# Kernel optimization log

Hardware: AMD Instinct MI355X
Metric: run time of the kernel (lower is better)

Reference implementation:

```python
import jax, jax.numpy as jnp
from jax import lax
import numpy as np

B, L, E, H = 4, 512, 1024, 128


def setup_inputs() -> dict:
    key = jax.random.key(0)
    k0, k1, k2, k3, k4, k5 = jax.random.split(key, 6)
    s = 1.0 / np.sqrt(E)
    return {
        "rec_emb": jax.random.normal(k0, (B, L, E), jnp.float32),
        "lig_emb": jax.random.normal(k1, (B, L, E), jnp.float32),
        "W1": jax.random.normal(k2, (E, H), jnp.float32) * s,
        "b1": jax.random.normal(k3, (H,), jnp.float32) * 0.01,
        "conv_w": jax.random.normal(k4, (1, H, 2, 2), jnp.float32) * (1.0 / np.sqrt(H * 4)),
        "conv_b": jax.random.normal(k5, (1,), jnp.float32) * 0.01,
    }


def reference(rec_emb, lig_emb, W1, b1, conv_w, conv_b):
    # shared fc: Linear -> ReLU (Dropout is identity in eval mode)
    rec_hid = jax.nn.relu(jnp.einsum("bie,eh->bih", rec_emb, W1) + b1)
    lig_hid = jax.nn.relu(jnp.einsum("bje,eh->bjh", lig_emb, W1) + b1)
    # outer-product bilinear map: bih,bjh->bijh, then tanh
    mat = jnp.tanh(rec_hid[:, :, None, :] * lig_hid[:, None, :, :])
    # permute to NCHW: (b, h, i, j)
    mat = jnp.transpose(mat, (0, 3, 1, 2))
    # Conv2d(H -> 1, kernel=2, padding=1): out spatial = L + 1
    y = lax.conv_general_dilated(
        mat, conv_w, window_strides=(1, 1), padding=[(1, 1), (1, 1)],
        dimension_numbers=("NCHW", "OIHW", "NCHW"),
    ) + conv_b[None, :, None, None]
    # MaxPool2d(kernel=2, stride=2), floor mode
    pooled = lax.reduce_window(
        y, -jnp.inf, lax.max,
        window_dimensions=(1, 1, 2, 2), window_strides=(1, 1, 2, 2),
        padding="VALID",
    )
    # global max over spatial dims -> (b, 1), sigmoid, flatten
    m = jnp.max(pooled, axis=(2, 3))
    return jax.nn.sigmoid(m).reshape(-1)
```

## Files before the change

### kernel.cpp

```cpp
#include <hip/hip_runtime.h>
#include <hip/hip_fp16.h>
#include <math.h>

#define BDIM 4
#define LDIM 512
#define EDIM 1024
#define HDIM 128
#define TILE 32
#define NT   16
#define K2   2.885390081777927f

typedef unsigned short ushort_t;
typedef __attribute__((ext_vector_type(8))) _Float16 half8;
typedef __attribute__((ext_vector_type(4))) float f32x4;

struct __align__(16) H8 { __half2 p[4]; };
union HU { H8 h; half8 v; };

__global__ __launch_bounds__(256) void gemm_direct(
    const float* __restrict__ rec, const float* __restrict__ lig,
    const float* __restrict__ W1, const float* __restrict__ b1,
    const float* __restrict__ cw, ushort_t* __restrict__ hid,
    ushort_t* __restrict__ wneg, float* __restrict__ wsumg) {
  if (blockIdx.x == 512) {
    __shared__ float wp[2][4];
    const int t = threadIdx.x;
    if (t < HDIM) {
      float4 w4 = *(const float4*)&cw[t * 4];
      _Float16 h0 = (_Float16)(-2.f * w4.x), h1 = (_Float16)(-2.f * w4.y);
      _Float16 h2 = (_Float16)(-2.f * w4.z), h3 = (_Float16)(-2.f * w4.w);
      wneg[0 * HDIM + t] = *(ushort_t*)&h0;
      wneg[1 * HDIM + t] = *(ushort_t*)&h1;
      wneg[2 * HDIM + t] = *(ushort_t*)&h2;
      wneg[3 * HDIM + t] = *(ushort_t*)&h3;
#pragma unroll
      for (int k = 4; k < 16; ++k) wneg[k * HDIM + t] = 0;
      float4 ws = w4;
#pragma unroll
      for (int off = 32; off > 0; off >>= 1) {
        ws.x += __shfl_down(ws.x, off, 64);
        ws.y += __shfl_down(ws.y, off, 64);
        ws.z += __shfl_down(ws.z, off, 64);
        ws.w += __shfl_down(ws.w, off, 64);
      }
      if ((t & 63) == 0) {
        wp[t >> 6][0] = ws.x; wp[t >> 6][1] = ws.y;
        wp[t >> 6][2] = ws.z; wp[t >> 6][3] = ws.w;
      }
    }
    __syncthreads();
    if (t < 4) wsumg[t] = wp[0][t] + wp[1][t];
    return;
  }

  const int gw = (int)blockIdx.x * 4 + (threadIdx.x >> 6);
  const int l = threadIdx.x & 63;
  const int strip = gw >> 3;
  const int nidx = gw & 7;
  const int r0 = strip * 16;
  const int m = l & 15, q = l >> 4;
  const float* arow = ((r0 < BDIM * LDIM)
                           ? rec + (size_t)r0 * EDIM
                           : lig + (size_t)(r0 - BDIM * LDIM) * EDIM) +
                      (size_t)m * EDIM + q * 8;
  const int col = nidx * 16 + m;
  const float* wcol = W1 + col;

  f32x4 acc = {0.f, 0.f, 0.f, 0.f};
  for (int blk = 0; blk < 8; ++blk) {
    float4 alo[4], ahi[4];
    float bw[4][8];
#pragma unroll
    for (int j = 0; j < 4; ++j) {
      const int k0 = (blk * 4 + j) * 32 + q * 8;
      alo[j] = *(const float4*)(arow + (blk * 4 + j) * 32);
      ahi[j] = *(const float4*)(arow + (blk * 4 + j) * 32 + 4);
#pragma unroll
      for (int kk = 0; kk < 8; ++kk)
        bw[j][kk] = wcol[(size_t)(k0 + kk) * HDIM];
    }
#pragma unroll
    for (int j = 0; j < 4; ++j) {
      HU au, bu;
      au.h.p[0] = __floats2half2_rn(alo[j].x, alo[j].y);
      au.h.p[1] = __floats2half2_rn(alo[j].z, alo[j].w);
      au.h.p[2] = __floats2half2_rn(ahi[j].x, ahi[j].y);
      au.h.p[3] = __floats2half2_rn(ahi[j].z, ahi[j].w);
      bu.h.p[0] = __floats2half2_rn(bw[j][0], bw[j][1]);
      bu.h.p[1] = __floats2half2_rn(bw[j][2], bw[j][3]);
      bu.h.p[2] = __floats2half2_rn(bw[j][4], bw[j][5]);
      bu.h.p[3] = __floats2half2_rn(bw[j][6], bw[j][7]);
      acc = __builtin_amdgcn_mfma_f32_16x16x32_f16(au.v, bu.v, acc, 0, 0, 0);
    }
  }
  const float scale = (r0 < BDIM * LDIM) ? -K2 : 1.0f;
  const float bias = b1[col];
#pragma unroll
  for (int r = 0; r < 4; ++r) {
    float v = fmaxf(acc[r] + bias, 0.f) * scale;
    ((_Float16*)hid)[(size_t)(r0 + q * 4 + r) * HDIM + col] = (_Float16)v;
  }
}

__global__ __launch_bounds__(256, 4) void bilinear_max(
    const ushort_t* __restrict__ hid, const ushort_t* __restrict__ wneg,
    const float* __restrict__ wsumg, const float* __restrict__ cw,
    const float* __restrict__ cb, float* __restrict__ partial) {
  __shared__ ushort_t rl[33][130];
  __shared__ ushort_t ll[33][130];
  __shared__ ushort_t sl4[33][34][4];
  __shared__ float wred[4];

  const int t = threadIdx.x;
  const int b = blockIdx.z;
  const int ib = (int)blockIdx.y * TILE - 1;
  const int jb = (int)blockIdx.x * TILE - 1;
  const int w = t >> 6, l = t & 63;
  const int q = l >> 4, c15 = l & 15;

  half8 wf[4];
#pragma unroll
  for (int c = 0; c < 4; ++c)
    wf[c] = *(const half8*)&wneg[c15 * HDIM + c * 32 + q * 8];
  const float wsum_v = (c15 < 4) ? wsumg[c15] : 0.f;

  H8 z;
  z.p[0] = z.p[1] = z.p[2] = z.p[3] = __floats2half2_rn(0.f, 0.f);
  for (int p = t; p < 66 * 16; p += 256) {
    int r = p >> 4, seg = (p & 15) * 8;
    if (r < 33) {
      int i = ib + r;
      H8 v = z;
      if (i >= 0) v = *(const H8*)&hid[((size_t)(b * LDIM + i)) * HDIM + seg];
      *(H8*)&rl[r][seg] = v;
    } else {
      int j = jb + (r - 33);
      H8 v = z;
      if (j >= 0) v = *(const H8*)&hid[((size_t)((BDIM + b) * LDIM + j)) * HDIM + seg];
      *(H8*)&ll[r - 33][seg] = v;
    }
  }
  __syncthreads();

  const __half2 E0 = __float2half2_rn(0.991381f);
  const __half2 E1 = __float2half2_rn(-0.818328f);
  const __half2 E2 = __float2half2_rn(0.333048f);
#define POLYG(U) __hmul2(U, __hfma2(U, __hfma2(U, E2, E1), E0))
#define GCHAIN(GU, RU, LU)                                                    \
  {                                                                           \
    __half2 u0 = h2exp2(__hmul2((RU).h.p[0], (LU).h.p[0]));                   \
    __half2 u1 = h2exp2(__hmul2((RU).h.p[1], (LU).h.p[1]));                   \
    __half2 u2 = h2exp2(__hmul2((RU).h.p[2], (LU).h.p[2]));                   \
    __half2 u3 = h2exp2(__hmul2((RU).h.p[3], (LU).h.p[3]));                   \
    (GU).h.p[0] = POLYG(u0);                                                  \
    (GU).h.p[1] = POLYG(u1);                                                  \
    (GU).h.p[2] = POLYG(u2);                                                  \
    (GU).h.p[3] = POLYG(u3);                                                  \
  }

#pragma unroll
  for (int hf = 0; hf < 2; ++hf) {
    const int jj0 = hf << 4;
    HU lu[4];
#pragma unroll
    for (int c = 0; c < 4; ++c)
      lu[c].v = *(const half8*)&ll[jj0 + c15][c * 32 + q * 8];
#pragma unroll
    for (int ii4 = 0; ii4 < 2; ++ii4) {
      const int ii = w * 8 + ii4 * 4;
      f32x4 a0 = {0.f, 0.f, 0.f, 0.f}, a1 = a0, a2 = a0, a3 = a0;
#pragma unroll
      for (int c = 0; c < 4; ++c) {
        HU r0, r1, r2, r3, g0, g1, g2, g3;
        r0.v = *(const half8*)&rl[ii + 0][c * 32 + q * 8];
        r1.v = *(const half8*)&rl[ii + 1][c * 32 + q * 8];
        r2.v = *(const half8*)&rl[ii + 2][c * 32 + q * 8];
        r3.v = *(const half8*)&rl[ii + 3][c * 32 + q * 8];
        GCHAIN(g0, r0, lu[c])
        GCHAIN(g1, r1, lu[c])
        GCHAIN(g2, r2, lu[c])
        GCHAIN(g3, r3, lu[c])
        a0 = __builtin_amdgcn_mfma_f32_16x16x32_f16(g0.v, wf[c], a0, 0, 0, 0);
        a1 = __builtin_amdgcn_mfma_f32_16x16x32_f16(g1.v, wf[c], a1, 0, 0, 0);
        a2 = __builtin_amdgcn_mfma_f32_16x16x32_f16(g2.v, wf[c], a2, 0, 0, 0);
        a3 = __builtin_amdgcn_mfma_f32_16x16x32_f16(g3.v, wf[c], a3, 0, 0, 0);
      }
      if (c15 < 4) {
#pragma unroll
        for (int r = 0; r < 4; ++r) {
          _Float16 h0 = (_Float16)(wsum_v + a0[r]);
          _Float16 h1 = (_Float16)(wsum_v + a1[r]);
          _Float16 h2 = (_Float16)(wsum_v + a2[r]);
          _Float16 h3 = (_Float16)(wsum_v + a3[r]);
          sl4[ii + 0][jj0 + q * 4 + r][c15] = *(ushort_t*)&h0;
          sl4[ii + 1][jj0 + q * 4 + r][c15] = *(ushort_t*)&h1;
          sl4[ii + 2][jj0 + q * 4 + r][c15] = *(ushort_t*)&h2;
          sl4[ii + 3][jj0 + q * 4 + r][c15] = *(ushort_t*)&h3;
        }
      }
    }
  }
#undef GCHAIN

  if (t < 130) {
    const int pr = t >> 1;
    const int hh = (t & 1) * 64;
    const int pi = (pr < 33) ? pr : 32;
    const int qj = (pr < 33) ? 32 : (pr - 33);
    float sa0 = 0.f, sa1 = 0.f, sa2 = 0.f, sa3 = 0.f;
    for (int h8 = hh; h8 < hh + 64; h8 += 8) {
      HU r8, l8;
      r8.v = *(const half8*)&rl[pi][h8];
      l8.v = *(const half8*)&ll[qj][h8];
#pragma unroll
      for (int j = 0; j < 4; ++j) {
        float2 pf = __half22float2(__hmul2(r8.h.p[j], l8.h.p[j]));
        float u0 = __builtin_amdgcn_exp2f(pf.x);
        float u1 = __builtin_amdgcn_exp2f(pf.y);
        float g0 = u0 * fmaf(u0, fmaf(u0, 0.333048f, -0.818328f), 0.991381f);
        float g1 = u1 * fmaf(u1, fmaf(u1, 0.333048f, -0.818328f), 0.991381f);
        float4 wa = *(const float4*)&cw[(h8 + 2 * j) * 4];
        float4 wb = *(const float4*)&cw[(h8 + 2 * j + 1) * 4];
        sa0 = fmaf(-2.f * g0, wa.x, fmaf(-2.f * g1, wb.x, sa0));
        sa1 = fmaf(-2.f * g0, wa.y, fmaf(-2.f * g1, wb.y, sa1));
        sa2 = fmaf(-2.f * g0, wa.z, fmaf(-2.f * g1, wb.z, sa2));
        sa3 = fmaf(-2.f * g0, wa.w, fmaf(-2.f * g1, wb.w, sa3));
      }
    }
    sa0 += __shfl_xor(sa0, 1, 64);
    sa1 += __shfl_xor(sa1, 1, 64);
    sa2 += __shfl_xor(sa2, 1, 64);
    sa3 += __shfl_xor(sa3, 1, 64);
    if ((t & 1) == 0) {
      _Float16 h0 = (_Float16)(wsumg[0] + sa0);
      _Float16 h1 = (_Float16)(wsumg[1] + sa1);
      _Float16 h2 = (_Float16)(wsumg[2] + sa2);
      _Float16 h3 = (_Float16)(wsumg[3] + sa3);
      sl4[pi][qj][0] = *(ushort_t*)&h0;
      sl4[pi][qj][1] = *(ushort_t*)&h1;
      sl4[pi][qj][2] = *(ushort_t*)&h2;
      sl4[pi][qj][3] = *(ushort_t*)&h3;
    }
  }
  __syncthreads();

  float m = -INFINITY;
  const float cbv = cb[0];
  for (int p = t; p < 1024; p += 256) {
    int jj = (p & 31) + 1, iy = (p >> 5) + 1;
    float v = cbv + (float)(*(const _Float16*)&sl4[iy - 1][jj - 1][0])
                  + (float)(*(const _Float16*)&sl4[iy - 1][jj][1])
                  + (float)(*(const _Float16*)&sl4[iy][jj - 1][2])
                  + (float)(*(const _Float16*)&sl4[iy][jj][3]);
    m = fmaxf(m, v);
  }
#pragma unroll
  for (int off = 32; off > 0; off >>= 1) m = fmaxf(m, __shfl_down(m, off, 64));
  if ((t & 63) == 0) wred[t >> 6] = m;
  __syncthreads();
  if (t == 0) {
    float mm = fmaxf(fmaxf(wred[0], wred[1]), fmaxf(wred[2], wred[3]));
    partial[((size_t)b * NT + blockIdx.y) * NT + blockIdx.x] = mm;
  }
}

__global__ __launch_bounds__(64) void finalize(const float* __restrict__ partial,
                                               float* __restrict__ out) {
  const int b = blockIdx.x, t = threadIdx.x;
  float m = -INFINITY;
  for (int p = t; p < NT * NT; p += 64) m = fmaxf(m, partial[b * NT * NT + p]);
#pragma unroll
  for (int off = 32; off > 0; off >>= 1) m = fmaxf(m, __shfl_down(m, off, 64));
  if (t == 0) out[b] = 1.f / (1.f + expf(-m));
}

extern "C" void kernel_launch(void* const* d_in, const int* in_sizes, int n_in,
                              void* d_out, int out_size, void* d_ws, size_t ws_size,
                              hipStream_t stream) {
  const float* rec = (const float*)d_in[0];
  const float* lig = (const float*)d_in[1];
  const float* W1  = (const float*)d_in[2];
  const float* b1  = (const float*)d_in[3];
  const float* cw  = (const float*)d_in[4];
  const float* cb  = (const float*)d_in[5];
  float* out = (float*)d_out;

  ushort_t* hid  = (ushort_t*)d_ws;
  float* partial = (float*)(hid + (size_t)2 * BDIM * LDIM * HDIM);
  ushort_t* wneg = (ushort_t*)(partial + NT * NT * BDIM);
  float* wsumg   = (float*)(wneg + 16 * HDIM);

  gemm_direct<<<dim3(513), 256, 0, stream>>>(rec, lig, W1, b1, cw, hid, wneg, wsumg);
  bilinear_max<<<dim3(NT, NT, BDIM), 256, 0, stream>>>(hid, wneg, wsumg, cw, cb, partial);
  finalize<<<dim3(BDIM), 64, 0, stream>>>(partial, out);
}
```

Baseline: 122.2 us.

## Pretranspose W1 to fp16 and shrink bilinear tile to 16x32 for occupancy

Adds a prep kernel that converts W1 to a transposed fp16 layout once per call, so the GEMM loads contiguous half8 vectors instead of eight strided fp32 loads per MFMA operand and drops the per-iteration conversions. The bilinear tile is reduced from 32x32 to 16x32 with launch bounds raised to 8 blocks per CU. The aim is more blocks and better occupancy, at the cost of more halo recomputation per output. This adds an extra kernel launch and reduces per-block reuse of the loaded row and column tiles.

New measurement: 128.1 us. 4.8% more time.

```diff
diff --git a/kernel.cpp b/kernel.cpp
--- a/kernel.cpp
+++ b/kernel.cpp
@@ -6,8 +6,10 @@
 #define LDIM 512
 #define EDIM 1024
 #define HDIM 128
-#define TILE 32
-#define NT   16
+#define TI   16
+#define TJ   32
+#define NTI  32
+#define NTJ  16
 #define K2   2.885390081777927f
 
 typedef unsigned short ushort_t;
@@ -17,14 +19,25 @@
 struct __align__(16) H8 { __half2 p[4]; };
 union HU { H8 h; half8 v; };
 
-__global__ __launch_bounds__(256) void gemm_direct(
-    const float* __restrict__ rec, const float* __restrict__ lig,
-    const float* __restrict__ W1, const float* __restrict__ b1,
-    const float* __restrict__ cw, ushort_t* __restrict__ hid,
-    ushort_t* __restrict__ wneg, float* __restrict__ wsumg) {
-  if (blockIdx.x == 512) {
+__global__ __launch_bounds__(256) void prep(
+    const float* __restrict__ W1, const float* __restrict__ cw,
+    ushort_t* __restrict__ w1t, ushort_t* __restrict__ wneg,
+    float* __restrict__ wsumg) {
+  const int t = threadIdx.x;
+  const int tid = (int)blockIdx.x * 256 + t;
+  const int col = tid & 127;
+  const int k8 = (tid >> 7) * 8;
+  HU hu;
+#pragma unroll
+  for (int e = 0; e < 4; ++e) {
+    float a = W1[(size_t)(k8 + 2 * e) * HDIM + col];
+    float b = W1[(size_t)(k8 + 2 * e + 1) * HDIM + col];
+    hu.h.p[e] = __floats2half2_rn(a, b);
+  }
+  *(half8*)&w1t[(size_t)col * EDIM + k8] = hu.v;
+
+  if (blockIdx.x == 0) {
     __shared__ float wp[2][4];
-    const int t = threadIdx.x;
     if (t < HDIM) {
       float4 w4 = *(const float4*)&cw[t * 4];
       _Float16 h0 = (_Float16)(-2.f * w4.x), h1 = (_Float16)(-2.f * w4.y);
@@ -50,9 +63,13 @@
     }
     __syncthreads();
     if (t < 4) wsumg[t] = wp[0][t] + wp[1][t];
-    return;
-  }
-
+  }
+}
+
+__global__ __launch_bounds__(256) void gemm_direct(
+    const float* __restrict__ rec, const float* __restrict__ lig,
+    const ushort_t* __restrict__ w1t, const float* __restrict__ b1,
+    ushort_t* __restrict__ hid) {
   const int gw = (int)blockIdx.x * 4 + (threadIdx.x >> 6);
   const int l = threadIdx.x & 63;
   const int strip = gw >> 3;
@@ -64,33 +81,27 @@
                            : lig + (size_t)(r0 - BDIM * LDIM) * EDIM) +
                       (size_t)m * EDIM + q * 8;
   const int col = nidx * 16 + m;
-  const float* wcol = W1 + col;
+  const ushort_t* wrow = w1t + (size_t)col * EDIM + q * 8;
 
   f32x4 acc = {0.f, 0.f, 0.f, 0.f};
+#pragma unroll 2
   for (int blk = 0; blk < 8; ++blk) {
     float4 alo[4], ahi[4];
-    float bw[4][8];
+    half8 bv[4];
 #pragma unroll
     for (int j = 0; j < 4; ++j) {
-      const int k0 = (blk * 4 + j) * 32 + q * 8;
       alo[j] = *(const float4*)(arow + (blk * 4 + j) * 32);
       ahi[j] = *(const float4*)(arow + (blk * 4 + j) * 32 + 4);
-#pragma unroll
-      for (int kk = 0; kk < 8; ++kk)
-        bw[j][kk] = wcol[(size_t)(k0 + kk) * HDIM];
+      bv[j] = *(const half8*)&wrow[(blk * 4 + j) * 32];
     }
 #pragma unroll
     for (int j = 0; j < 4; ++j) {
-      HU au, bu;
+      HU au;
       au.h.p[0] = __floats2half2_rn(alo[j].x, alo[j].y);
       au.h.p[1] = __floats2half2_rn(alo[j].z, alo[j].w);
       au.h.p[2] = __floats2half2_rn(ahi[j].x, ahi[j].y);
       au.h.p[3] = __floats2half2_rn(ahi[j].z, ahi[j].w);
-      bu.h.p[0] = __floats2half2_rn(bw[j][0], bw[j][1]);
-      bu.h.p[1] = __floats2half2_rn(bw[j][2], bw[j][3]);
-      bu.h.p[2] = __floats2half2_rn(bw[j][4], bw[j][5]);
-      bu.h.p[3] = __floats2half2_rn(bw[j][6], bw[j][7]);
-      acc = __builtin_amdgcn_mfma_f32_16x16x32_f16(au.v, bu.v, acc, 0, 0, 0);
+      acc = __builtin_amdgcn_mfma_f32_16x16x32_f16(au.v, bv[j], acc, 0, 0, 0);
     }
   }
   const float scale = (r0 < BDIM * LDIM) ? -K2 : 1.0f;
@@ -102,19 +113,19 @@
   }
 }
 
-__global__ __launch_bounds__(256, 4) void bilinear_max(
+__global__ __launch_bounds__(256, 8) void bilinear_max(
     const ushort_t* __restrict__ hid, const ushort_t* __restrict__ wneg,
     const float* __restrict__ wsumg, const float* __restrict__ cw,
     const float* __restrict__ cb, float* __restrict__ partial) {
-  __shared__ ushort_t rl[33][130];
-  __shared__ ushort_t ll[33][130];
-  __shared__ ushort_t sl4[33][34][4];
+  __shared__ ushort_t rl[TI + 1][130];
+  __shared__ ushort_t ll[TJ + 1][130];
+  __shared__ ushort_t sl4[TI + 1][TJ + 2][4];
   __shared__ float wred[4];
 
   const int t = threadIdx.x;
   const int b = blockIdx.z;
-  const int ib = (int)blockIdx.y * TILE - 1;
-  const int jb = (int)blockIdx.x * TILE - 1;
+  const int ib = (int)blockIdx.y * TI - 1;
+  const int jb = (int)blockIdx.x * TJ - 1;
   const int w = t >> 6, l = t & 63;
   const int q = l >> 4, c15 = l & 15;
 
@@ -126,18 +137,18 @@
 
   H8 z;
   z.p[0] = z.p[1] = z.p[2] = z.p[3] = __floats2half2_rn(0.f, 0.f);
-  for (int p = t; p < 66 * 16; p += 256) {
+  for (int p = t; p < (TI + TJ + 2) * 16; p += 256) {
     int r = p >> 4, seg = (p & 15) * 8;
-    if (r < 33) {
+    if (r < TI + 1) {
       int i = ib + r;
       H8 v = z;
       if (i >= 0) v = *(const H8*)&hid[((size_t)(b * LDIM + i)) * HDIM + seg];
       *(H8*)&rl[r][seg] = v;
     } else {
-      int j = jb + (r - 33);
+      int j = jb + (r - (TI + 1));
       H8 v = z;
       if (j >= 0) v = *(const H8*)&hid[((size_t)((BDIM + b) * LDIM + j)) * HDIM + seg];
-      *(H8*)&ll[r - 33][seg] = v;
+      *(H8*)&ll[r - (TI + 1)][seg] = v;
     }
   }
   __syncthreads();
@@ -165,48 +176,46 @@
 #pragma unroll
     for (int c = 0; c < 4; ++c)
       lu[c].v = *(const half8*)&ll[jj0 + c15][c * 32 + q * 8];
-#pragma unroll
-    for (int ii4 = 0; ii4 < 2; ++ii4) {
-      const int ii = w * 8 + ii4 * 4;
-      f32x4 a0 = {0.f, 0.f, 0.f, 0.f}, a1 = a0, a2 = a0, a3 = a0;
-#pragma unroll
-      for (int c = 0; c < 4; ++c) {
-        HU r0, r1, r2, r3, g0, g1, g2, g3;
-        r0.v = *(const half8*)&rl[ii + 0][c * 32 + q * 8];
-        r1.v = *(const half8*)&rl[ii + 1][c * 32 + q * 8];
-        r2.v = *(const half8*)&rl[ii + 2][c * 32 + q * 8];
-        r3.v = *(const half8*)&rl[ii + 3][c * 32 + q * 8];
-        GCHAIN(g0, r0, lu[c])
-        GCHAIN(g1, r1, lu[c])
-        GCHAIN(g2, r2, lu[c])
-        GCHAIN(g3, r3, lu[c])
-        a0 = __builtin_amdgcn_mfma_f32_16x16x32_f16(g0.v, wf[c], a0, 0, 0, 0);
-        a1 = __builtin_amdgcn_mfma_f32_16x16x32_f16(g1.v, wf[c], a1, 0, 0, 0);
-        a2 = __builtin_amdgcn_mfma_f32_16x16x32_f16(g2.v, wf[c], a2, 0, 0, 0);
-        a3 = __builtin_amdgcn_mfma_f32_16x16x32_f16(g3.v, wf[c], a3, 0, 0, 0);
+    const int ii = w * 4;
+    f32x4 a0 = {0.f, 0.f, 0.f, 0.f}, a1 = a0, a2 = a0, a3 = a0;
+#pragma unroll
+    for (int c = 0; c < 4; ++c) {
+      HU r0, r1, r2, r3, g0, g1, g2, g3;
+      r0.v = *(const half8*)&rl[ii + 0][c * 32 + q * 8];
+      r1.v = *(const half8*)&rl[ii + 1][c * 32 + q * 8];
+      r2.v = *(const half8*)&rl[ii + 2][c * 32 + q * 8];
+      r3.v = *(const half8*)&rl[ii + 3][c * 32 + q * 8];
+      GCHAIN(g0, r0, lu[c])
+      GCHAIN(g1, r1, lu[c])
+      GCHAIN(g2, r2, lu[c])
+      GCHAIN(g3, r3, lu[c])
+      a0 = __builtin_amdgcn_mfma_f32_16x16x32_f16(g0.v, wf[c], a0, 0, 0, 0);
+      a1 = __builtin_amdgcn_mfma_f32_16x16x32_f16(g1.v, wf[c], a1, 0, 0, 0);
+      a2 = __builtin_amdgcn_mfma_f32_16x16x32_f16(g2.v, wf[c], a2, 0, 0, 0);
+      a3 = __builtin_amdgcn_mfma_f32_16x16x32_f16(g3.v, wf[c], a3, 0, 0, 0);
+    }
+    if (c15 < 4) {
+#pragma unroll
+      for (int r = 0; r < 4; ++r) {
+        _Float16 h0 = (_Float16)(wsum_v + a0[r]);
+        _Float16 h1 = (_Float16)(wsum_v + a1[r]);
+        _Float16 h2 = (_Float16)(wsum_v + a2[r]);
+        _Float16 h3 = (_Float16)(wsum_v + a3[r]);
+        sl4[ii + 0][jj0 + q * 4 + r][c15] = *(ushort_t*)&h0;
+        sl4[ii + 1][jj0 + q * 4 + r][c15] = *(ushort_t*)&h1;
+        sl4[ii + 2][jj0 + q * 4 + r][c15] = *(ushort_t*)&h2;
+        sl4[ii + 3][jj0 + q * 4 + r][c15] = *(ushort_t*)&h3;
       }
-      if (c15 < 4) {
-#pragma unroll
-        for (int r = 0; r < 4; ++r) {
-          _Float16 h0 = (_Float16)(wsum_v + a0[r]);
-          _Float16 h1 = (_Float16)(wsum_v + a1[r]);
-          _Float16 h2 = (_Float16)(wsum_v + a2[r]);
-          _Float16 h3 = (_Float16)(wsum_v + a3[r]);
-          sl4[ii + 0][jj0 + q * 4 + r][c15] = *(ushort_t*)&h0;
-          sl4[ii + 1][jj0 + q * 4 + r][c15] = *(ushort_t*)&h1;
-          sl4[ii + 2][jj0 + q * 4 + r][c15] = *(ushort_t*)&h2;
-          sl4[ii + 3][jj0 + q * 4 + r][c15] = *(ushort_t*)&h3;
-        }
-      }
     }
   }
 #undef GCHAIN
-
-  if (t < 130) {
+#undef POLYG
+
+  if (t < 98) {
     const int pr = t >> 1;
     const int hh = (t & 1) * 64;
-    const int pi = (pr < 33) ? pr : 32;
-    const int qj = (pr < 33) ? 32 : (pr - 33);
+    const int pi = (pr < TI + 1) ? pr : TI;
+    const int qj = (pr < TI + 1) ? TJ : (pr - (TI + 1));
     float sa0 = 0.f, sa1 = 0.f, sa2 = 0.f, sa3 = 0.f;
     for (int h8 = hh; h8 < hh + 64; h8 += 8) {
       HU r8, l8;
@@ -246,7 +255,7 @@
 
   float m = -INFINITY;
   const float cbv = cb[0];
-  for (int p = t; p < 1024; p += 256) {
+  for (int p = t; p < TI * TJ; p += 256) {
     int jj = (p & 31) + 1, iy = (p >> 5) + 1;
     float v = cbv + (float)(*(const _Float16*)&sl4[iy - 1][jj - 1][0])
                   + (float)(*(const _Float16*)&sl4[iy - 1][jj][1])
@@ -260,7 +269,7 @@
   __syncthreads();
   if (t == 0) {
     float mm = fmaxf(fmaxf(wred[0], wred[1]), fmaxf(wred[2], wred[3]));
-    partial[((size_t)b * NT + blockIdx.y) * NT + blockIdx.x] = mm;
+    partial[((size_t)b * NTI + blockIdx.y) * NTJ + blockIdx.x] = mm;
   }
 }
 
@@ -268,7 +277,7 @@
                                                float* __restrict__ out) {
   const int b = blockIdx.x, t = threadIdx.x;
   float m = -INFINITY;
-  for (int p = t; p < NT * NT; p += 64) m = fmaxf(m, partial[b * NT * NT + p]);
+  for (int p = t; p < NTI * NTJ; p += 64) m = fmaxf(m, partial[b * NTI * NTJ + p]);
 #pragma unroll
   for (int off = 32; off > 0; off >>= 1) m = fmaxf(m, __shfl_down(m, off, 64));
   if (t == 0) out[b] = 1.f / (1.f + expf(-m));
@@ -287,10 +296,12 @@
 
   ushort_t* hid  = (ushort_t*)d_ws;
   float* partial = (float*)(hid + (size_t)2 * BDIM * LDIM * HDIM);
-  ushort_t* wneg = (ushort_t*)(partial + NT * NT * BDIM);
+  ushort_t* wneg = (ushort_t*)(partial + NTI * NTJ * BDIM);
   float* wsumg   = (float*)(wneg + 16 * HDIM);
-
-  gemm_direct<<<dim3(513), 256, 0, stream>>>(rec, lig, W1, b1, cw, hid, wneg, wsumg);
-  bilinear_max<<<dim3(NT, NT, BDIM), 256, 0, stream>>>(hid, wneg, wsumg, cw, cb, partial);
+  ushort_t* w1t  = (ushort_t*)(wsumg + 4);
+
+  prep<<<dim3(64), 256, 0, stream>>>(W1, cw, w1t, wneg, wsumg);
+  gemm_direct<<<dim3(512), 256, 0, stream>>>(rec, lig, w1t, b1, hid);
+  bilinear_max<<<dim3(NTJ, NTI, BDIM), 256, 0, stream>>>(hid, wneg, wsumg, cw, cb, partial);
   finalize<<<dim3(BDIM), 64, 0, stream>>>(partial, out);
 }
```

## Split GEMM K across warps and double bilinear block threads

Applied to the files above, without the earlier changes.

The projection GEMM now gives each block one 16x16 output tile and splits the K=1024 reduction across its four warps, combining the partial sums through shared memory. That quadruples the grid to 2048+1 blocks and shortens each warp's serial MFMA chain. The bilinear kernel moves to 512 threads per block, so each warp handles 4 rows instead of 8, and the border computation is split four ways with one packed 8-byte store. The trade is more parallelism and latency hiding against a shared-memory reduction and a barrier in the GEMM, plus register pressure from the higher launch bounds.

Result: slower. 128.1 us (+4.8%).

```diff
diff --git a/kernel.cpp b/kernel.cpp
--- a/kernel.cpp
+++ b/kernel.cpp
@@ -16,13 +16,14 @@
 
 struct __align__(16) H8 { __half2 p[4]; };
 union HU { H8 h; half8 v; };
-
-__global__ __launch_bounds__(256) void gemm_direct(
+struct __align__(8) US4 { ushort_t u[4]; };
+
+__global__ __launch_bounds__(256, 8) void gemm_direct(
     const float* __restrict__ rec, const float* __restrict__ lig,
     const float* __restrict__ W1, const float* __restrict__ b1,
     const float* __restrict__ cw, ushort_t* __restrict__ hid,
     ushort_t* __restrict__ wneg, float* __restrict__ wsumg) {
-  if (blockIdx.x == 512) {
+  if (blockIdx.x == 2048) {
     __shared__ float wp[2][4];
     const int t = threadIdx.x;
     if (t < HDIM) {
@@ -53,63 +54,66 @@
     return;
   }
 
-  const int gw = (int)blockIdx.x * 4 + (threadIdx.x >> 6);
-  const int l = threadIdx.x & 63;
-  const int strip = gw >> 3;
-  const int nidx = gw & 7;
+  __shared__ float red[4][64][4];
+  const int t = threadIdx.x;
+  const int w = t >> 6, l = t & 63;
+  const int m = l & 15, q = l >> 4;
+  const int strip = (int)blockIdx.x >> 3;
+  const int nidx = (int)blockIdx.x & 7;
   const int r0 = strip * 16;
-  const int m = l & 15, q = l >> 4;
   const float* arow = ((r0 < BDIM * LDIM)
                            ? rec + (size_t)r0 * EDIM
                            : lig + (size_t)(r0 - BDIM * LDIM) * EDIM) +
-                      (size_t)m * EDIM + q * 8;
+                      (size_t)m * EDIM;
   const int col = nidx * 16 + m;
   const float* wcol = W1 + col;
+  const int ks = w * 256;
 
   f32x4 acc = {0.f, 0.f, 0.f, 0.f};
+#pragma unroll 2
   for (int blk = 0; blk < 8; ++blk) {
-    float4 alo[4], ahi[4];
-    float bw[4][8];
-#pragma unroll
-    for (int j = 0; j < 4; ++j) {
-      const int k0 = (blk * 4 + j) * 32 + q * 8;
-      alo[j] = *(const float4*)(arow + (blk * 4 + j) * 32);
-      ahi[j] = *(const float4*)(arow + (blk * 4 + j) * 32 + 4);
-#pragma unroll
-      for (int kk = 0; kk < 8; ++kk)
-        bw[j][kk] = wcol[(size_t)(k0 + kk) * HDIM];
-    }
-#pragma unroll
-    for (int j = 0; j < 4; ++j) {
-      HU au, bu;
-      au.h.p[0] = __floats2half2_rn(alo[j].x, alo[j].y);
-      au.h.p[1] = __floats2half2_rn(alo[j].z, alo[j].w);
-      au.h.p[2] = __floats2half2_rn(ahi[j].x, ahi[j].y);
-      au.h.p[3] = __floats2half2_rn(ahi[j].z, ahi[j].w);
-      bu.h.p[0] = __floats2half2_rn(bw[j][0], bw[j][1]);
-      bu.h.p[1] = __floats2half2_rn(bw[j][2], bw[j][3]);
-      bu.h.p[2] = __floats2half2_rn(bw[j][4], bw[j][5]);
-      bu.h.p[3] = __floats2half2_rn(bw[j][6], bw[j][7]);
-      acc = __builtin_amdgcn_mfma_f32_16x16x32_f16(au.v, bu.v, acc, 0, 0, 0);
-    }
-  }
-  const float scale = (r0 < BDIM * LDIM) ? -K2 : 1.0f;
-  const float bias = b1[col];
-#pragma unroll
-  for (int r = 0; r < 4; ++r) {
-    float v = fmaxf(acc[r] + bias, 0.f) * scale;
-    ((_Float16*)hid)[(size_t)(r0 + q * 4 + r) * HDIM + col] = (_Float16)v;
+    const int k0 = ks + blk * 32 + q * 8;
+    float4 alo = *(const float4*)(arow + k0);
+    float4 ahi = *(const float4*)(arow + k0 + 4);
+    float bw[8];
+#pragma unroll
+    for (int kk = 0; kk < 8; ++kk) bw[kk] = wcol[(size_t)(k0 + kk) * HDIM];
+    HU au, bu;
+    au.h.p[0] = __floats2half2_rn(alo.x, alo.y);
+    au.h.p[1] = __floats2half2_rn(alo.z, alo.w);
+    au.h.p[2] = __floats2half2_rn(ahi.x, ahi.y);
+    au.h.p[3] = __floats2half2_rn(ahi.z, ahi.w);
+    bu.h.p[0] = __floats2half2_rn(bw[0], bw[1]);
+    bu.h.p[1] = __floats2half2_rn(bw[2], bw[3]);
+    bu.h.p[2] = __floats2half2_rn(bw[4], bw[5]);
+    bu.h.p[3] = __floats2half2_rn(bw[6], bw[7]);
+    acc = __builtin_amdgcn_mfma_f32_16x16x32_f16(au.v, bu.v, acc, 0, 0, 0);
+  }
+  *(f32x4*)&red[w][l][0] = acc;
+  __syncthreads();
+  if (w == 0) {
+    f32x4 s0 = *(const f32x4*)&red[0][l][0];
+    f32x4 s1 = *(const f32x4*)&red[1][l][0];
+    f32x4 s2 = *(const f32x4*)&red[2][l][0];
+    f32x4 s3 = *(const f32x4*)&red[3][l][0];
+    const float scale = (r0 < BDIM * LDIM) ? -K2 : 1.0f;
+    const float bias = b1[col];
+#pragma unroll
+    for (int r = 0; r < 4; ++r) {
+      float v = fmaxf(s0[r] + s1[r] + s2[r] + s3[r] + bias, 0.f) * scale;
+      ((_Float16*)hid)[(size_t)(r0 + q * 4 + r) * HDIM + col] = (_Float16)v;
+    }
   }
 }
 
-__global__ __launch_bounds__(256, 4) void bilinear_max(
+__global__ __launch_bounds__(512, 8) void bilinear_max(
     const ushort_t* __restrict__ hid, const ushort_t* __restrict__ wneg,
     const float* __restrict__ wsumg, const float* __restrict__ cw,
     const float* __restrict__ cb, float* __restrict__ partial) {
   __shared__ ushort_t rl[33][130];
   __shared__ ushort_t ll[33][130];
   __shared__ ushort_t sl4[33][34][4];
-  __shared__ float wred[4];
+  __shared__ float wred[8];
 
   const int t = threadIdx.x;
   const int b = blockIdx.z;
@@ -126,7 +130,7 @@
 
   H8 z;
   z.p[0] = z.p[1] = z.p[2] = z.p[3] = __floats2half2_rn(0.f, 0.f);
-  for (int p = t; p < 66 * 16; p += 256) {
+  for (int p = t; p < 66 * 16; p += 512) {
     int r = p >> 4, seg = (p & 15) * 8;
     if (r < 33) {
       int i = ib + r;
@@ -165,50 +169,49 @@
 #pragma unroll
     for (int c = 0; c < 4; ++c)
       lu[c].v = *(const half8*)&ll[jj0 + c15][c * 32 + q * 8];
-#pragma unroll
-    for (int ii4 = 0; ii4 < 2; ++ii4) {
-      const int ii = w * 8 + ii4 * 4;
-      f32x4 a0 = {0.f, 0.f, 0.f, 0.f}, a1 = a0, a2 = a0, a3 = a0;
-#pragma unroll
-      for (int c = 0; c < 4; ++c) {
-        HU r0, r1, r2, r3, g0, g1, g2, g3;
-        r0.v = *(const half8*)&rl[ii + 0][c * 32 + q * 8];
-        r1.v = *(const half8*)&rl[ii + 1][c * 32 + q * 8];
-        r2.v = *(const half8*)&rl[ii + 2][c * 32 + q * 8];
-        r3.v = *(const half8*)&rl[ii + 3][c * 32 + q * 8];
-        GCHAIN(g0, r0, lu[c])
-        GCHAIN(g1, r1, lu[c])
-        GCHAIN(g2, r2, lu[c])
-        GCHAIN(g3, r3, lu[c])
-        a0 = __builtin_amdgcn_mfma_f32_16x16x32_f16(g0.v, wf[c], a0, 0, 0, 0);
-        a1 = __builtin_amdgcn_mfma_f32_16x16x32_f16(g1.v, wf[c], a1, 0, 0, 0);
-        a2 = __builtin_amdgcn_mfma_f32_16x16x32_f16(g2.v, wf[c], a2, 0, 0, 0);
-        a3 = __builtin_amdgcn_mfma_f32_16x16x32_f16(g3.v, wf[c], a3, 0, 0, 0);
+    const int ii = w * 4;
+    f32x4 a0 = {0.f, 0.f, 0.f, 0.f}, a1 = a0, a2 = a0, a3 = a0;
+#pragma unroll
+    for (int c = 0; c < 4; ++c) {
+      HU r0, r1, r2, r3, g0, g1, g2, g3;
+      r0.v = *(const half8*)&rl[ii + 0][c * 32 + q * 8];
+      r1.v = *(const half8*)&rl[ii + 1][c * 32 + q * 8];
+      r2.v = *(const half8*)&rl[ii + 2][c * 32 + q * 8];
+      r3.v = *(const half8*)&rl[ii + 3][c * 32 + q * 8];
+      GCHAIN(g0, r0, lu[c])
+      GCHAIN(g1, r1, lu[c])
+      GCHAIN(g2, r2, lu[c])
+      GCHAIN(g3, r3, lu[c])
+      a0 = __builtin_amdgcn_mfma_f32_16x16x32_f16(g0.v, wf[c], a0, 0, 0, 0);
+      a1 = __builtin_amdgcn_mfma_f32_16x16x32_f16(g1.v, wf[c], a1, 0, 0, 0);
+      a2 = __builtin_amdgcn_mfma_f32_16x16x32_f16(g2.v, wf[c], a2, 0, 0, 0);
+      a3 = __builtin_amdgcn_mfma_f32_16x16x32_f16(g3.v, wf[c], a3, 0, 0, 0);
+    }
+    if (c15 < 4) {
+#pragma unroll
+      for (int r = 0; r < 4; ++r) {
+        _Float16 h0 = (_Float16)(wsum_v + a0[r]);
+        _Float16 h1 = (_Float16)(wsum_v + a1[r]);
+        _Float16 h2 = (_Float16)(wsum_v + a2[r]);
+        _Float16 h3 = (_Float16)(wsum_v + a3[r]);
+        sl4[ii + 0][jj0 + q * 4 + r][c15] = *(ushort_t*)&h0;
+        sl4[ii + 1][jj0 + q * 4 + r][c15] = *(ushort_t*)&h1;
+        sl4[ii + 2][jj0 + q * 4 + r][c15] = *(ushort_t*)&h2;
+        sl4[ii + 3][jj0 + q * 4 + r][c15] = *(ushort_t*)&h3;
       }
-      if (c15 < 4) {
-#pragma unroll
-        for (int r = 0; r < 4; ++r) {
-          _Float16 h0 = (_Float16)(wsum_v + a0[r]);
-          _Float16 h1 = (_Float16)(wsum_v + a1[r]);
-          _Float16 h2 = (_Float16)(wsum_v + a2[r]);
-          _Float16 h3 = (_Float16)(wsum_v + a3[r]);
-          sl4[ii + 0][jj0 + q * 4 + r][c15] = *(ushort_t*)&h0;
-          sl4[ii + 1][jj0 + q * 4 + r][c15] = *(ushort_t*)&h1;
-          sl4[ii + 2][jj0 + q * 4 + r][c15] = *(ushort_t*)&h2;
-          sl4[ii + 3][jj0 + q * 4 + r][c15] = *(ushort_t*)&h3;
-        }
-      }
     }
   }
 #undef GCHAIN
-
-  if (t < 130) {
-    const int pr = t >> 1;
-    const int hh = (t & 1) * 64;
+#undef POLYG
+
+  if (t < 260) {
+    const int pr = t >> 2;
+    const int o = t & 3;
     const int pi = (pr < 33) ? pr : 32;
     const int qj = (pr < 33) ? 32 : (pr - 33);
     float sa0 = 0.f, sa1 = 0.f, sa2 = 0.f, sa3 = 0.f;
-    for (int h8 = hh; h8 < hh + 64; h8 += 8) {
+    const int hb = o * 32;
+    for (int h8 = hb; h8 < hb + 32; h8 += 8) {
       HU r8, l8;
       r8.v = *(const half8*)&rl[pi][h8];
       l8.v = *(const half8*)&ll[qj][h8];
@@ -231,22 +234,26 @@
     sa1 += __shfl_xor(sa1, 1, 64);
     sa2 += __shfl_xor(sa2, 1, 64);
     sa3 += __shfl_xor(sa3, 1, 64);
-    if ((t & 1) == 0) {
+    sa0 += __shfl_xor(sa0, 2, 64);
+    sa1 += __shfl_xor(sa1, 2, 64);
+    sa2 += __shfl_xor(sa2, 2, 64);
+    sa3 += __shfl_xor(sa3, 2, 64);
+    if (o == 0) {
       _Float16 h0 = (_Float16)(wsumg[0] + sa0);
       _Float16 h1 = (_Float16)(wsumg[1] + sa1);
       _Float16 h2 = (_Float16)(wsumg[2] + sa2);
       _Float16 h3 = (_Float16)(wsumg[3] + sa3);
-      sl4[pi][qj][0] = *(ushort_t*)&h0;
-      sl4[pi][qj][1] = *(ushort_t*)&h1;
-      sl4[pi][qj][2] = *(ushort_t*)&h2;
-      sl4[pi][qj][3] = *(ushort_t*)&h3;
+      US4 s;
+      s.u[0] = *(ushort_t*)&h0; s.u[1] = *(ushort_t*)&h1;
+      s.u[2] = *(ushort_t*)&h2; s.u[3] = *(ushort_t*)&h3;
+      *(US4*)&sl4[pi][qj][0] = s;
     }
   }
   __syncthreads();
 
   float m = -INFINITY;
   const float cbv = cb[0];
-  for (int p = t; p < 1024; p += 256) {
+  for (int p = t; p < TILE * TILE; p += 512) {
     int jj = (p & 31) + 1, iy = (p >> 5) + 1;
     float v = cbv + (float)(*(const _Float16*)&sl4[iy - 1][jj - 1][0])
                   + (float)(*(const _Float16*)&sl4[iy - 1][jj][1])
@@ -259,7 +266,9 @@
   if ((t & 63) == 0) wred[t >> 6] = m;
   __syncthreads();
   if (t == 0) {
-    float mm = fmaxf(fmaxf(wred[0], wred[1]), fmaxf(wred[2], wred[3]));
+    float mm = wred[0];
+#pragma unroll
+    for (int i = 1; i < 8; ++i) mm = fmaxf(mm, wred[i]);
     partial[((size_t)b * NT + blockIdx.y) * NT + blockIdx.x] = mm;
   }
 }
@@ -290,7 +299,7 @@
   ushort_t* wneg = (ushort_t*)(partial + NT * NT * BDIM);
   float* wsumg   = (float*)(wneg + 16 * HDIM);
 
-  gemm_direct<<<dim3(513), 256, 0, stream>>>(rec, lig, W1, b1, cw, hid, wneg, wsumg);
-  bilinear_max<<<dim3(NT, NT, BDIM), 256, 0, stream>>>(hid, wneg, wsumg, cw, cb, partial);
+  gemm_direct<<<dim3(2049), 256, 0, stream>>>(rec, lig, W1, b1, cw, hid, wneg, wsumg);
+  bilinear_max<<<dim3(NT, NT, BDIM), 512, 0, stream>>>(hid, wneg, wsumg, cw, cb, partial);
   finalize<<<dim3(BDIM), 64, 0, stream>>>(partial, out);
 }
```
